# Optimization experiments

Measured on AMD Instinct MI355X. Metric: run time of the kernel, lower is better.

Reference implementation:

```python
import jax, jax.numpy as jnp
import numpy as np
from jax import lax

B, T, V, E, H = 256, 512, 128, 64, 256


def lstm_cell(x, h, c, Wih, Whh, bih, bhh):
    # PyTorch gate order: i, f, g, o
    gates = x @ Wih.T + h @ Whh.T + bih + bhh
    i, f, g, o = jnp.split(gates, 4, axis=-1)
    c_new = jax.nn.sigmoid(f) * c + jax.nn.sigmoid(i) * jnp.tanh(g)
    h_new = jax.nn.sigmoid(o) * jnp.tanh(c_new)
    return h_new, c_new


def setup_inputs() -> dict:
    key = jax.random.key(0)
    ks = jax.random.split(key, 16)
    s = 0.05
    emb = jax.random.normal(ks[1], (V, E), jnp.float32) * s
    emb = emb.at[0].set(0.0)  # padding_idx=0
    return {
        "x": jax.random.randint(ks[0], (B, T), 0, V),
        "emb": emb,
        "Wih_e": jax.random.normal(ks[2], (4 * H, E), jnp.float32) * s,
        "Whh_e": jax.random.normal(ks[3], (4 * H, H), jnp.float32) * s,
        "bih_e": jax.random.normal(ks[4], (4 * H,), jnp.float32) * s,
        "bhh_e": jax.random.normal(ks[5], (4 * H,), jnp.float32) * s,
        "Wq": jax.random.normal(ks[6], (H, H), jnp.float32) * s,
        "Wk": jax.random.normal(ks[7], (H, H), jnp.float32) * s,
        "v": jax.random.normal(ks[8], (H,), jnp.float32) * s,
        "Wih_d": jax.random.normal(ks[9], (4 * H, E + H), jnp.float32) * s,
        "Whh_d": jax.random.normal(ks[10], (4 * H, H), jnp.float32) * s,
        "bih_d": jax.random.normal(ks[11], (4 * H,), jnp.float32) * s,
        "bhh_d": jax.random.normal(ks[12], (4 * H,), jnp.float32) * s,
        "Wfc": jax.random.normal(ks[13], (V, H), jnp.float32) * s,
        "bfc": jax.random.normal(ks[14], (V,), jnp.float32) * s,
    }


def reference(x, emb, Wih_e, Whh_e, bih_e, bhh_e, Wq, Wk, v,
              Wih_d, Whh_d, bih_d, bhh_d, Wfc, bfc):
    Bx = x.shape[0]
    embedded = emb[x]                          # (B, T, E)  (dropout in eval mode = identity)
    emb_tbE = embedded.transpose(1, 0, 2)      # (T, B, E)

    # ---- Encoder LSTM ----
    h0 = jnp.zeros((Bx, H), embedded.dtype)
    c0 = jnp.zeros((Bx, H), embedded.dtype)

    def enc_step(carry, x_t):
        h, c = carry
        h, c = lstm_cell(x_t, h, c, Wih_e, Whh_e, bih_e, bhh_e)
        return (h, c), h

    (h_n, c_n), enc_seq = lax.scan(enc_step, (h0, c0), emb_tbE)
    enc_out = enc_seq.transpose(1, 0, 2)       # (B, T, H)

    # ---- Attention precompute ----
    keys_proj = enc_out @ Wk.T                 # (B, T, H)
    pad_mask = (x == 0)                        # (B, T)

    # ---- Decoder loop (teacher forcing) ----
    def dec_step(carry, emb_t):
        h, c = carry
        q = h @ Wq.T                                        # (B, H)
        energy = jnp.tanh(q[:, None, :] + keys_proj) @ v    # (B, T)
        energy = jnp.where(pad_mask, -1e9, energy)
        w = jax.nn.softmax(energy, axis=-1)
        context = jnp.einsum('bt,bth->bh', w, enc_out)      # (B, H)
        dec_in = jnp.concatenate([emb_t, context], axis=-1)  # (B, E+H)
        h, c = lstm_cell(dec_in, h, c, Wih_d, Whh_d, bih_d, bhh_d)
        return (h, c), h

    (h_f, c_f), dec_seq = lax.scan(dec_step, (h_n, c_n), emb_tbE)
    logits = dec_seq.transpose(1, 0, 2) @ Wfc.T + bfc       # (B, T, V)
    return logits, h_f, c_f
```

## Files before the change

kernel.cpp:

```cpp
#include <hip/hip_runtime.h>
#include <hip/hip_bf16.h>
#include <stdint.h>

#define NB 256
#define NT 512
#define NV 128
#define NE 64
#define NH 256

typedef __fp16 h2t __attribute__((ext_vector_type(2)));

__device__ __forceinline__ float lo_bf(unsigned u){ return __uint_as_float(u << 16); }
__device__ __forceinline__ float hi_bf(unsigned u){ return __uint_as_float(u & 0xffff0000u); }
__device__ __forceinline__ unsigned short f2us(float f){
  unsigned u = __float_as_uint(f);
  unsigned r = u + 0x7fffu + ((u >> 16) & 1u);
  return (unsigned short)(r >> 16);
}
__device__ __forceinline__ float sigm(float x){
  return __builtin_amdgcn_rcpf(1.f + __expf(-x));
}
__device__ __forceinline__ float ftanh(float xx){
  float a = fabsf(xx);
  a = fminf(a, 9.f);
  float e = __expf(2.f * a);
  float r = __builtin_amdgcn_rcpf(e + 1.f);
  float t = (e - 1.f) * r;
  return copysignf(t, xx);
}
__device__ __forceinline__ unsigned pkf16(float a, float b){
  h2t h = __builtin_amdgcn_cvt_pkrtz(a, b);
  unsigned u; __builtin_memcpy(&u, &h, 4); return u;
}
__device__ __forceinline__ float fdot2(unsigned a, unsigned b, float c){
#if __has_builtin(__builtin_amdgcn_fdot2)
  h2t A, B; __builtin_memcpy(&A, &a, 4); __builtin_memcpy(&B, &b, 4);
  return __builtin_amdgcn_fdot2(A, B, c, false);
#else
  h2t A, B; __builtin_memcpy(&A, &a, 4); __builtin_memcpy(&B, &b, 4);
  return c + (float)A.x*(float)B.x + (float)A.y*(float)B.y;
#endif
}

__global__ __launch_bounds__(256, 1)
void prep_kernel(const float* __restrict__ Wq, const float* __restrict__ Wfc,
                 const float* __restrict__ Wihd, const float* __restrict__ Whhd,
                 const float* __restrict__ Wihe, const float* __restrict__ Whhe,
                 const float* __restrict__ Wk,
                 unsigned* __restrict__ Wq4, unsigned* __restrict__ Wfc4,
                 unsigned* __restrict__ Wihd4, unsigned* __restrict__ Whhd4,
                 unsigned* __restrict__ Wihe4, unsigned* __restrict__ Whhe4,
                 unsigned* __restrict__ Wke4)
{
  const int blk = blockIdx.x, tid = threadIdx.x;
  if (blk < 64){
    int k2p = blk;
    #pragma unroll
    for (int l = 0; l < 2; ++l){
      int i = l*256 + tid, c = i>>1, j = i&1, k = 4*k2p + 2*j;
      Wq4[k2p*512 + i] = pkf16(Wq[c*256 + k], Wq[c*256 + k + 1]);
    }
  } else if (blk < 128){
    int k2p = blk - 64;
    int c = tid>>1, j = tid&1, k = 4*k2p + 2*j;
    Wfc4[k2p*256 + tid] = pkf16(Wfc[c*256 + k], Wfc[c*256 + k + 1]);
  } else if (blk < 208){
    int k2p = blk - 128;
    #pragma unroll
    for (int l = 0; l < 8; ++l){
      int i = l*256 + tid, g = i>>1, j = i&1, k = 4*k2p + 2*j;
      Wihd4[(size_t)k2p*2048 + i] = pkf16(Wihd[g*320 + k], Wihd[g*320 + k + 1]);
    }
  } else if (blk < 272){
    int k2p = blk - 208;
    #pragma unroll
    for (int l = 0; l < 8; ++l){
      int i = l*256 + tid, g = i>>1, j = i&1, k = 4*k2p + 2*j;
      Whhd4[(size_t)k2p*2048 + i] = pkf16(Whhd[g*256 + k], Whhd[g*256 + k + 1]);
    }
  } else if (blk < 288){
    int k2p = blk - 272;
    #pragma unroll
    for (int l = 0; l < 8; ++l){
      int i = l*256 + tid, g = i>>1, j = i&1, k = 4*k2p + 2*j;
      Wihe4[(size_t)k2p*2048 + i] = pkf16(Wihe[g*64 + k], Wihe[g*64 + k + 1]);
    }
  } else if (blk < 352){
    int k2p = blk - 288;
    #pragma unroll
    for (int l = 0; l < 8; ++l){
      int i = l*256 + tid, g = i>>1, j = i&1, k = 4*k2p + 2*j;
      Whhe4[(size_t)k2p*2048 + i] = pkf16(Whhe[g*256 + k], Whhe[g*256 + k + 1]);
    }
  } else {
    int k2p = blk - 352;
    #pragma unroll
    for (int l = 0; l < 2; ++l){
      int i = l*256 + tid, c = i>>1, j = i&1, k = 4*k2p + 2*j;
      Wke4[k2p*512 + i] = pkf16(Wk[c*256 + k], Wk[c*256 + k + 1]);
    }
  }
}

__global__ __launch_bounds__(256, 1)
void tr_kernel(const unsigned short* __restrict__ keys_n, unsigned short* __restrict__ keys_t)
{
  __shared__ unsigned short tile[64][68];
  const int blk = blockIdx.x, tid = threadIdx.x;
  const int b  = blk >> 5;
  const int tt = (blk >> 2) & 7;
  const int hh = blk & 3;
  const int t0 = tt*64, h0 = hh*64;

  #pragma unroll
  for (int i = 0; i < 4; ++i){
    int idx = tid + i*256;
    int t = idx >> 4, h4 = (idx & 15)*4;
    uint2 u = *(const uint2*)(keys_n + ((size_t)b*NT + t0 + t)*NH + h0 + h4);
    *(uint2*)&tile[t][h4] = u;
  }
  __syncthreads();
  #pragma unroll
  for (int i = 0; i < 4; ++i){
    int idx = tid + i*256;
    int h = idx >> 4, t4 = (idx & 15)*4;
    unsigned short a = tile[t4+0][h], bb = tile[t4+1][h], cc = tile[t4+2][h], dd = tile[t4+3][h];
    uint2 u; u.x = (unsigned)a | ((unsigned)bb << 16); u.y = (unsigned)cc | ((unsigned)dd << 16);
    *(uint2*)(keys_t + ((size_t)b*NH + h0 + h)*NT + t0 + t4) = u;
  }
}

__global__ __launch_bounds__(1024, 1)
void enc_kernel(const int* __restrict__ x, const float* __restrict__ emb,
                const unsigned* __restrict__ Wihe4, const unsigned* __restrict__ Whhe4,
                const float* __restrict__ bih, const float* __restrict__ bhh,
                const unsigned* __restrict__ Wke4,
                unsigned short* __restrict__ enc_out, unsigned short* __restrict__ keys_n,
                float* __restrict__ g_h, float* __restrict__ g_c)
{
  const int tid = threadIdx.x;
  const int b0  = blockIdx.x * 2;

  __shared__ unsigned sH2[2][128];
  __shared__ unsigned sXe2[2][32];
  __shared__ float sG[2][1024];
  __shared__ float sBias[1024];
  __shared__ float sKP[1024];
  __shared__ uint8_t sXi[2][512];

  sBias[tid] = bih[tid] + bhh[tid];
  { int r = tid >> 9; sXi[r][tid & 511] = (uint8_t)x[(b0 + r)*NT + (tid & 511)]; }
  if (tid < 256) sH2[tid>>7][tid&127] = 0u;
  __syncthreads();
  if (tid < 64){
    int r = tid>>5, p = tid&31, idx = sXi[r][0];
    sXe2[r][p] = pkf16(emb[idx*NE + 2*p], emb[idx*NE + 2*p + 1]);
  }
  float creg = 0.f, hl = 0.f;
  __syncthreads();

  for (int t = 0; t < NT; ++t){
    {
      const int g = tid;
      float a0 = sBias[g], a1 = a0;
      const unsigned* Wi = Wihe4 + g*2;
      #pragma unroll 4
      for (int p = 0; p < 16; ++p){
        uint2 w = *(const uint2*)(Wi + (size_t)p*2048);
        a0 = fdot2(sXe2[0][2*p], w.x, a0); a0 = fdot2(sXe2[0][2*p+1], w.y, a0);
        a1 = fdot2(sXe2[1][2*p], w.x, a1); a1 = fdot2(sXe2[1][2*p+1], w.y, a1);
      }
      const unsigned* Wh = Whhe4 + g*2;
      #pragma unroll 4
      for (int p = 0; p < 64; ++p){
        uint2 w = *(const uint2*)(Wh + (size_t)p*2048);
        a0 = fdot2(sH2[0][2*p], w.x, a0); a0 = fdot2(sH2[0][2*p+1], w.y, a0);
        a1 = fdot2(sH2[1][2*p], w.x, a1); a1 = fdot2(sH2[1][2*p+1], w.y, a1);
      }
      sG[0][g] = a0; sG[1][g] = a1;
    }
    if (t > 0){
      const int r = tid>>9, half = (tid>>8)&1, c = tid&255;
      float kp = 0.f;
      const unsigned* Wk4 = Wke4 + c*2;
      #pragma unroll 4
      for (int p = 0; p < 32; ++p){
        int k2p = half*32 + p;
        uint2 w = *(const uint2*)(Wk4 + k2p*512);
        kp = fdot2(sH2[r][2*k2p], w.x, kp);
        kp = fdot2(sH2[r][2*k2p+1], w.y, kp);
      }
      sKP[tid] = kp;
    }
    __syncthreads();
    if (tid < 512){
      const int r = tid>>8, cc = tid&255;
      float gi = sigm (sG[r][cc]);
      float gf = sigm (sG[r][256+cc]);
      float gg = ftanh(sG[r][512+cc]);
      float go = sigm (sG[r][768+cc]);
      float cn = gf*creg + gi*gg;
      float hn = go*ftanh(cn);
      creg = cn; hl = hn;
      enc_out[((size_t)(b0+r)*NT + t)*NH + cc] = f2us(hn);
      float hb = __shfl_down(hn, 1, 64);
      if (!(cc & 1)) sH2[r][cc>>1] = pkf16(hn, hb);
      if (tid < 64 && (t+1) < NT){
        int r2 = tid>>5, p = tid&31, idx = sXi[r2][t+1];
        sXe2[r2][p] = pkf16(emb[idx*NE + 2*p], emb[idx*NE + 2*p + 1]);
      }
    } else if (t > 0){
      const int r = (tid>>8)&1, c = tid&255;
      float kv = sKP[(r<<9) + c] + sKP[(r<<9) + 256 + c];
      keys_n[((size_t)(b0+r)*NT + (t-1))*NH + c] = f2us(kv);
    }
    __syncthreads();
  }
  {
    const int r = tid>>9, half = (tid>>8)&1, c = tid&255;
    float kp = 0.f;
    const unsigned* Wk4 = Wke4 + c*2;
    #pragma unroll 4
    for (int p = 0; p < 32; ++p){
      int k2p = half*32 + p;
      uint2 w = *(const uint2*)(Wk4 + k2p*512);
      kp = fdot2(sH2[r][2*k2p], w.x, kp);
      kp = fdot2(sH2[r][2*k2p+1], w.y, kp);
    }
    sKP[tid] = kp;
  }
  __syncthreads();
  if (tid >= 512){
    const int r = (tid>>8)&1, c = tid&255;
    float kv = sKP[(r<<9) + c] + sKP[(r<<9) + 256 + c];
    keys_n[((size_t)(b0+r)*NT + (NT-1))*NH + c] = f2us(kv);
  } else {
    const int r = tid>>8, cc = tid&255;
    g_h[(b0+r)*NH + cc] = hl;
    g_c[(b0+r)*NH + cc] = creg;
  }
}

__global__ __launch_bounds__(1024, 1)
void dec_kernel(const int* __restrict__ x, const float* __restrict__ emb,
                const unsigned* __restrict__ Wq4, const float* __restrict__ vvec,
                const unsigned* __restrict__ Wihd4, const unsigned* __restrict__ Whhd4,
                const float* __restrict__ bih, const float* __restrict__ bhh,
                const unsigned short* __restrict__ enc_out, const unsigned short* __restrict__ keys_t,
                const float* __restrict__ g_h, const float* __restrict__ g_c,
                unsigned* __restrict__ h2_hist, float* __restrict__ out_h, float* __restrict__ out_c)
{
  const int tid = threadIdx.x;
  const int b   = blockIdx.x;

  __shared__ float sTMP[4096];
  __shared__ float sWp[512];
  __shared__ float sRed[8];
  __shared__ float sQ2[256];
  __shared__ unsigned sH2[128];
  __shared__ unsigned sCtx2[128];
  __shared__ unsigned sXe2[32];
  __shared__ float sG[1024];
  __shared__ float sBiasD[1024];
  __shared__ float sVm2[256];
  __shared__ float sVs[8];
  __shared__ uint8_t sXi[512];

  sBiasD[tid] = bih[tid] + bhh[tid];
  if (tid < 256) sVm2[tid] = -2.f * vvec[tid];
  if (tid < 512) sXi[tid] = (uint8_t)x[b*NT + tid];
  if (tid < 128) sH2[tid] = pkf16(g_h[b*NH + 2*tid], g_h[b*NH + 2*tid + 1]);
  if (tid < 8){
    float s = 0.f;
    #pragma unroll
    for (int j = 0; j < 32; ++j) s += vvec[tid*32 + j];
    sVs[tid] = s;
  }
  float creg = (tid < 256) ? g_c[b*NH + tid] : 0.f;
  float hl = 0.f;
  const float CLN = 2.885390081777927f;
  __syncthreads();

  for (int t = 0; t < NT; ++t){
    {
      const int c = tid & 255, kq = tid >> 8;
      float a = 0.f;
      const unsigned* Wp = Wq4 + c*2;
      #pragma unroll 4
      for (int p = 0; p < 16; ++p){
        int k2p = kq*16 + p;
        uint2 w = *(const uint2*)(Wp + k2p*512);
        a = fdot2(sH2[2*k2p], w.x, a);
        a = fdot2(sH2[2*k2p+1], w.y, a);
      }
      sTMP[kq*256 + c] = a;
    }
    __syncthreads();
    if (tid < 256){
      float qv = sTMP[tid] + sTMP[256 + tid] + sTMP[512 + tid] + sTMP[768 + tid];
      sQ2[tid] = CLN * qv;
    } else if (tid < 288){
      int p = tid - 256, idx = sXi[t];
      sXe2[p] = pkf16(emb[idx*NE + 2*p], emb[idx*NE + 2*p + 1]);
    }
    __syncthreads();
    {
      const int kh = tid >> 7, sp = tid & 127;
      const unsigned short* ktp = keys_t + ((size_t)b*NH + kh*32)*NT + sp*4;
      float e0 = sVs[kh], e1 = e0, e2 = e0, e3 = e0;
      #pragma unroll 4
      for (int kk = 0; kk < 32; ++kk){
        uint2 u = *(const uint2*)(ktp + (size_t)kk*NT);
        float q2 = sQ2[kh*32 + kk];
        float vm = sVm2[kh*32 + kk];
        float r0 = __builtin_amdgcn_rcpf(1.f + exp2f(fmaf(CLN, lo_bf(u.x), q2)));
        float r1 = __builtin_amdgcn_rcpf(1.f + exp2f(fmaf(CLN, hi_bf(u.x), q2)));
        float r2 = __builtin_amdgcn_rcpf(1.f + exp2f(fmaf(CLN, lo_bf(u.y), q2)));
        float r3 = __builtin_amdgcn_rcpf(1.f + exp2f(fmaf(CLN, hi_bf(u.y), q2)));
        e0 = fmaf(vm, r0, e0); e1 = fmaf(vm, r1, e1);
        e2 = fmaf(vm, r2, e2); e3 = fmaf(vm, r3, e3);
      }
      *(float4*)(sTMP + kh*512 + sp*4) = make_float4(e0,e1,e2,e3);
    }
    __syncthreads();
    if (tid < 512){
      float e = sTMP[tid]      + sTMP[512+tid]  + sTMP[1024+tid] + sTMP[1536+tid]
              + sTMP[2048+tid] + sTMP[2560+tid] + sTMP[3072+tid] + sTMP[3584+tid];
      float w = (sXi[tid] == 0) ? 0.f : __expf(e);
      sWp[tid] = w;
      float s = w;
      #pragma unroll
      for (int off = 32; off > 0; off >>= 1) s += __shfl_down(s, off, 64);
      if ((tid & 63) == 0) sRed[tid >> 6] = s;
    }
    __syncthreads();
    {
      const int sc = tid >> 6;
      const int kc = tid & 63;
      const unsigned short* ep = enc_out + ((size_t)b*NT + sc*32)*NH + kc*4;
      float a0=0.f, a1=0.f, a2=0.f, a3=0.f;
      #pragma unroll 8
      for (int ss = 0; ss < 32; ++ss){
        float w = sWp[sc*32 + ss];
        uint2 u = *(const uint2*)(ep + (size_t)ss*NH);
        a0 += w*lo_bf(u.x); a1 += w*hi_bf(u.x);
        a2 += w*lo_bf(u.y); a3 += w*hi_bf(u.y);
      }
      *(float4*)(sTMP + sc*256 + kc*4) = make_float4(a0,a1,a2,a3);
    }
    __syncthreads();
    if (tid < 256){
      float den = sRed[0]+sRed[1]+sRed[2]+sRed[3]+sRed[4]+sRed[5]+sRed[6]+sRed[7];
      float rden = (den > 0.f) ? (1.f/den) : 0.f;
      float cs = 0.f;
      #pragma unroll
      for (int p = 0; p < 16; ++p) cs += sTMP[p*256 + tid];
      float cv = cs * rden;
      float cb = __shfl_down(cv, 1, 64);
      if (!(tid & 1)) sCtx2[tid>>1] = pkf16(cv, cb);
    }
    __syncthreads();
    {
      const int g = tid;
      float a = sBiasD[g];
      const unsigned* Wi = Wihd4 + g*2;
      #pragma unroll 4
      for (int p = 0; p < 16; ++p){
        uint2 w = *(const uint2*)(Wi + (size_t)p*2048);
        a = fdot2(sXe2[2*p], w.x, a); a = fdot2(sXe2[2*p+1], w.y, a);
      }
      #pragma unroll 4
      for (int p = 0; p < 64; ++p){
        uint2 w = *(const uint2*)(Wi + (size_t)(16+p)*2048);
        a = fdot2(sCtx2[2*p], w.x, a); a = fdot2(sCtx2[2*p+1], w.y, a);
      }
      const unsigned* Wh = Whhd4 + g*2;
      #pragma unroll 4
      for (int p = 0; p < 64; ++p){
        uint2 w = *(const uint2*)(Wh + (size_t)p*2048);
        a = fdot2(sH2[2*p], w.x, a); a = fdot2(sH2[2*p+1], w.y, a);
      }
      sG[g] = a;
    }
    __syncthreads();
    if (tid < 256){
      float gi = sigm (sG[tid]);
      float gf = sigm (sG[256 + tid]);
      float gg = ftanh(sG[512 + tid]);
      float go = sigm (sG[768 + tid]);
      float cn = gf*creg + gi*gg;
      float hn = go*ftanh(cn);
      creg = cn; hl = hn;
      float hb = __shfl_down(hn, 1, 64);
      if (!(tid & 1)){
        unsigned hp = pkf16(hn, hb);
        sH2[tid>>1] = hp;
        h2_hist[((size_t)b*NT + t)*128 + (tid>>1)] = hp;
      }
    }
    __syncthreads();
  }

  if (tid < 256){
    out_h[b*NH + tid] = hl;
    out_c[b*NH + tid] = creg;
  }
}

__global__ __launch_bounds__(256, 1)
void fc_kernel(const unsigned* __restrict__ h2_hist, const unsigned* __restrict__ Wfc4,
               const float* __restrict__ bfc, float* __restrict__ logits)
{
  __shared__ unsigned sHH[1024];
  const int tid = threadIdx.x;
  const size_t row0 = (size_t)blockIdx.x * 8;
  #pragma unroll
  for (int l = 0; l < 4; ++l) sHH[l*256 + tid] = h2_hist[row0*128 + l*256 + tid];
  __syncthreads();
  const int r = tid >> 7, v = tid & 127;
  float bv = bfc[v];
  float a0 = bv, a1 = bv, a2 = bv, a3 = bv;
  const unsigned* Wp = Wfc4 + v*2;
  #pragma unroll 4
  for (int k2p = 0; k2p < 64; ++k2p){
    uint2 w = *(const uint2*)(Wp + k2p*256);
    int k2 = 2*k2p;
    a0 = fdot2(sHH[(r  )*128 + k2], w.x, a0); a0 = fdot2(sHH[(r  )*128 + k2+1], w.y, a0);
    a1 = fdot2(sHH[(r+2)*128 + k2], w.x, a1); a1 = fdot2(sHH[(r+2)*128 + k2+1], w.y, a1);
    a2 = fdot2(sHH[(r+4)*128 + k2], w.x, a2); a2 = fdot2(sHH[(r+4)*128 + k2+1], w.y, a2);
    a3 = fdot2(sHH[(r+6)*128 + k2], w.x, a3); a3 = fdot2(sHH[(r+6)*128 + k2+1], w.y, a3);
  }
  logits[(row0 + r    )*NV + v] = a0;
  logits[(row0 + r + 2)*NV + v] = a1;
  logits[(row0 + r + 4)*NV + v] = a2;
  logits[(row0 + r + 6)*NV + v] = a3;
}

extern "C" void kernel_launch(void* const* d_in, const int* in_sizes, int n_in,
                              void* d_out, int out_size, void* d_ws, size_t ws_size,
                              hipStream_t stream)
{
  (void)in_sizes; (void)n_in; (void)out_size; (void)ws_size;
  const int*   x    = (const int*)  d_in[0];
  const float* emb  = (const float*)d_in[1];
  const float* Wihe = (const float*)d_in[2];
  const float* Whhe = (const float*)d_in[3];
  const float* bihe = (const float*)d_in[4];
  const float* bhhe = (const float*)d_in[5];
  const float* Wq   = (const float*)d_in[6];
  const float* Wk   = (const float*)d_in[7];
  const float* vv   = (const float*)d_in[8];
  const float* Wihd = (const float*)d_in[9];
  const float* Whhd = (const float*)d_in[10];
  const float* bihd = (const float*)d_in[11];
  const float* bhhd = (const float*)d_in[12];
  const float* Wfc  = (const float*)d_in[13];
  const float* bfc  = (const float*)d_in[14];

  char* ws = (char*)d_ws;
  const size_t M64 = 67108864;
  unsigned short* enc   = (unsigned short*)(ws);
  unsigned short* keysn = (unsigned short*)(ws + M64);
  unsigned short* keyst = (unsigned short*)(ws + 2*M64);
  unsigned* h2_hist     = (unsigned*)(ws + M64);
  float* g_h = (float*)(ws + 3*M64);
  float* g_c = g_h + NB*NH;
  unsigned* Wq4   = (unsigned*)(g_c + NB*NH);
  unsigned* Wfc4  = Wq4   + 64*512;
  unsigned* Wihd4 = Wfc4  + 64*256;
  unsigned* Whhd4 = Wihd4 + 80*2048;
  unsigned* Wihe4 = Whhd4 + 64*2048;
  unsigned* Whhe4 = Wihe4 + 16*2048;
  unsigned* Wke4  = Whhe4 + 64*2048;

  float* out_logits = (float*)d_out;
  float* out_h = out_logits + (size_t)NB*NT*NV;
  float* out_c = out_h + NB*NH;

  prep_kernel<<<dim3(416), dim3(256), 0, stream>>>(
      Wq, Wfc, Wihd, Whhd, Wihe, Whhe, Wk,
      Wq4, Wfc4, Wihd4, Whhd4, Wihe4, Whhe4, Wke4);
  enc_kernel<<<dim3(128), dim3(1024), 0, stream>>>(
      x, emb, Wihe4, Whhe4, bihe, bhhe, Wke4, enc, keysn, g_h, g_c);
  tr_kernel<<<dim3(8192), dim3(256), 0, stream>>>(keysn, keyst);
  dec_kernel<<<dim3(256), dim3(1024), 0, stream>>>(
      x, emb, Wq4, vv, Wihd4, Whhd4, bihd, bhhd,
      enc, keyst, g_h, g_c, h2_hist, out_h, out_c);
  fc_kernel<<<dim3(16384), dim3(256), 0, stream>>>(h2_hist, Wfc4, bfc, out_logits);
}
```

Baseline: 25.66 ms.

## Pin part of attention keys in LDS and prefetch enc_out into registers

The decoder kernel now copies the first 96 of 256 hidden rows of this batch's transposed attention keys into dynamic shared memory (96 KB) once, before the time loop. Threads handling those rows read keys from LDS instead of global memory on every step. It also issues loads for half of each thread's enc_out context rows before the energy computation, so that global latency overlaps with the tanh/exp work. The cost is much higher LDS use and 16 extra uint2 registers per thread, which can raise register pressure at 1024 threads per block and limit occupancy.

Result: slower. 28.57 ms (+11.3%).

```diff
diff --git a/kernel.cpp b/kernel.cpp
--- a/kernel.cpp
+++ b/kernel.cpp
@@ -253,6 +253,8 @@
   const int tid = threadIdx.x;
   const int b   = blockIdx.x;
 
+  extern __shared__ unsigned short sKpin[];
+
   __shared__ float sTMP[4096];
   __shared__ float sWp[512];
   __shared__ float sRed[8];
@@ -276,12 +278,19 @@
     for (int j = 0; j < 32; ++j) s += vvec[tid*32 + j];
     sVs[tid] = s;
   }
+  {
+    const unsigned* src = (const unsigned*)(keys_t + (size_t)b*NH*NT);
+    unsigned* dst = (unsigned*)sKpin;
+    #pragma unroll
+    for (int i = 0; i < 24; ++i) dst[tid + i*1024] = src[tid + i*1024];
+  }
   float creg = (tid < 256) ? g_c[b*NH + tid] : 0.f;
   float hl = 0.f;
   const float CLN = 2.885390081777927f;
   __syncthreads();
 
   for (int t = 0; t < NT; ++t){
+    uint2 pf[16];
     {
       const int c = tid & 255, kq = tid >> 8;
       float a = 0.f;
@@ -305,20 +314,42 @@
     }
     __syncthreads();
     {
+      const int sc = tid >> 6, kc = tid & 63;
+      const unsigned short* ep = enc_out + ((size_t)b*NT + sc*32)*NH + kc*4;
+      #pragma unroll
+      for (int ss = 0; ss < 16; ++ss) pf[ss] = *(const uint2*)(ep + (size_t)ss*NH);
+    }
+    {
       const int kh = tid >> 7, sp = tid & 127;
-      const unsigned short* ktp = keys_t + ((size_t)b*NH + kh*32)*NT + sp*4;
       float e0 = sVs[kh], e1 = e0, e2 = e0, e3 = e0;
-      #pragma unroll 4
-      for (int kk = 0; kk < 32; ++kk){
-        uint2 u = *(const uint2*)(ktp + (size_t)kk*NT);
-        float q2 = sQ2[kh*32 + kk];
-        float vm = sVm2[kh*32 + kk];
-        float r0 = __builtin_amdgcn_rcpf(1.f + exp2f(fmaf(CLN, lo_bf(u.x), q2)));
-        float r1 = __builtin_amdgcn_rcpf(1.f + exp2f(fmaf(CLN, hi_bf(u.x), q2)));
-        float r2 = __builtin_amdgcn_rcpf(1.f + exp2f(fmaf(CLN, lo_bf(u.y), q2)));
-        float r3 = __builtin_amdgcn_rcpf(1.f + exp2f(fmaf(CLN, hi_bf(u.y), q2)));
-        e0 = fmaf(vm, r0, e0); e1 = fmaf(vm, r1, e1);
-        e2 = fmaf(vm, r2, e2); e3 = fmaf(vm, r3, e3);
+      if (kh < 3){
+        const unsigned short* ktp = sKpin + (size_t)(kh*32)*NT + sp*4;
+        #pragma unroll 4
+        for (int kk = 0; kk < 32; ++kk){
+          uint2 u = *(const uint2*)(ktp + (size_t)kk*NT);
+          float q2 = sQ2[kh*32 + kk];
+          float vm = sVm2[kh*32 + kk];
+          float r0 = __builtin_amdgcn_rcpf(1.f + exp2f(fmaf(CLN, lo_bf(u.x), q2)));
+          float r1 = __builtin_amdgcn_rcpf(1.f + exp2f(fmaf(CLN, hi_bf(u.x), q2)));
+          float r2 = __builtin_amdgcn_rcpf(1.f + exp2f(fmaf(CLN, lo_bf(u.y), q2)));
+          float r3 = __builtin_amdgcn_rcpf(1.f + exp2f(fmaf(CLN, hi_bf(u.y), q2)));
+          e0 = fmaf(vm, r0, e0); e1 = fmaf(vm, r1, e1);
+          e2 = fmaf(vm, r2, e2); e3 = fmaf(vm, r3, e3);
+        }
+      } else {
+        const unsigned short* ktp = keys_t + ((size_t)b*NH + kh*32)*NT + sp*4;
+        #pragma unroll 4
+        for (int kk = 0; kk < 32; ++kk){
+          uint2 u = *(const uint2*)(ktp + (size_t)kk*NT);
+          float q2 = sQ2[kh*32 + kk];
+          float vm = sVm2[kh*32 + kk];
+          float r0 = __builtin_amdgcn_rcpf(1.f + exp2f(fmaf(CLN, lo_bf(u.x), q2)));
+          float r1 = __builtin_amdgcn_rcpf(1.f + exp2f(fmaf(CLN, hi_bf(u.x), q2)));
+          float r2 = __builtin_amdgcn_rcpf(1.f + exp2f(fmaf(CLN, lo_bf(u.y), q2)));
+          float r3 = __builtin_amdgcn_rcpf(1.f + exp2f(fmaf(CLN, hi_bf(u.y), q2)));
+          e0 = fmaf(vm, r0, e0); e1 = fmaf(vm, r1, e1);
+          e2 = fmaf(vm, r2, e2); e3 = fmaf(vm, r3, e3);
+        }
       }
       *(float4*)(sTMP + kh*512 + sp*4) = make_float4(e0,e1,e2,e3);
     }
@@ -339,8 +370,15 @@
       const int kc = tid & 63;
       const unsigned short* ep = enc_out + ((size_t)b*NT + sc*32)*NH + kc*4;
       float a0=0.f, a1=0.f, a2=0.f, a3=0.f;
-      #pragma unroll 8
-      for (int ss = 0; ss < 32; ++ss){
+      #pragma unroll
+      for (int ss = 0; ss < 16; ++ss){
+        float w = sWp[sc*32 + ss];
+        uint2 u = pf[ss];
+        a0 += w*lo_bf(u.x); a1 += w*hi_bf(u.x);
+        a2 += w*lo_bf(u.y); a3 += w*hi_bf(u.y);
+      }
+      #pragma unroll 4
+      for (int ss = 16; ss < 32; ++ss){
         float w = sWp[sc*32 + ss];
         uint2 u = *(const uint2*)(ep + (size_t)ss*NH);
         a0 += w*lo_bf(u.x); a1 += w*hi_bf(u.x);
@@ -477,13 +515,21 @@
   float* out_h = out_logits + (size_t)NB*NT*NV;
   float* out_c = out_h + NB*NH;
 
+  const int dynLds = 96 * 512 * 2;
+  static int attrSet = 0;
+  if (!attrSet){
+    hipFuncSetAttribute(reinterpret_cast<const void*>(dec_kernel),
+                        hipFuncAttributeMaxDynamicSharedMemorySize, dynLds);
+    attrSet = 1;
+  }
+
   prep_kernel<<<dim3(416), dim3(256), 0, stream>>>(
       Wq, Wfc, Wihd, Whhd, Wihe, Whhe, Wk,
       Wq4, Wfc4, Wihd4, Whhd4, Wihe4, Whhe4, Wke4);
   enc_kernel<<<dim3(128), dim3(1024), 0, stream>>>(
       x, emb, Wihe4, Whhe4, bihe, bhhe, Wke4, enc, keysn, g_h, g_c);
   tr_kernel<<<dim3(8192), dim3(256), 0, stream>>>(keysn, keyst);
-  dec_kernel<<<dim3(256), dim3(1024), 0, stream>>>(
+  dec_kernel<<<dim3(256), dim3(1024), dynLds, stream>>>(
       x, emb, Wq4, vv, Wihd4, Whhd4, bihd, bhhd,
       enc, keyst, g_h, g_c, h2_hist, out_h, out_c);
   fc_kernel<<<dim3(16384), dim3(256), 0, stream>>>(h2_hist, Wfc4, bfc, out_logits);
```
